# Optimization experiments

Hardware: AMD Instinct MI355X
Metric: run time of the kernel (lower is better)

The kernel has to match this reference:

```python
import jax, jax.numpy as jnp
import numpy as np

B, L, D, N, H = 2, 2048, 1024, 16, 64  # batch, seq, d_model, heads, head_dim


def setup_inputs() -> dict:
    key = jax.random.key(0)
    k_x, k_qkv, k_proj = jax.random.split(key, 3)
    x = jax.random.normal(k_x, (B, L, D), dtype=jnp.float32)
    # RoPE table (L, H//2, 2) holding (cos, sin) per position/frequency
    inv_freq = 1.0 / (10000.0 ** (jnp.arange(H // 2, dtype=jnp.float32) / (H // 2)))
    ang = jnp.arange(L, dtype=jnp.float32)[:, None] * inv_freq[None, :]  # (L, H//2)
    rope = jnp.stack([jnp.cos(ang), jnp.sin(ang)], axis=-1)  # (L, H//2, 2)
    mask = jnp.tril(jnp.ones((L, L), dtype=bool))[None, None]  # (1,1,L,L) causal
    w_qkv = jax.random.normal(k_qkv, (D, 3 * D), dtype=jnp.float32) * 0.02
    w_proj = jax.random.normal(k_proj, (D, D), dtype=jnp.float32) * 0.02
    return {"x": x, "rope": rope, "mask": mask, "w_qkv": w_qkv, "w_proj": w_proj}


def _apply_rope(t, rope):
    # t: (B, L, N, H), rope: (L, H//2, 2)
    b, l, n, h = t.shape
    tp = t.reshape(b, l, n, h // 2, 2)
    cos = rope[None, :, None, :, 0]  # (1, L, 1, H//2)
    sin = rope[None, :, None, :, 1]
    t0, t1 = tp[..., 0], tp[..., 1]
    out = jnp.stack([t0 * cos - t1 * sin, t0 * sin + t1 * cos], axis=-1)
    return out.reshape(b, l, n, h)


def reference(x, rope, mask, w_qkv, w_proj):
    b, l, d = x.shape
    h = rope.shape[1] * 2
    n = d // h
    qkv = x @ w_qkv  # (b, l, 3d)
    q, k, v = jnp.split(qkv, 3, axis=2)
    q = _apply_rope(q.reshape(b, l, n, h), rope)
    k = _apply_rope(k.reshape(b, l, n, h), rope)
    v = v.reshape(b, l, n, h)
    scale = 1.0 / jnp.sqrt(jnp.asarray(h, dtype=x.dtype))
    scores = jnp.einsum('blnh,bmnh->bnlm', q, k) * scale  # (b, n, l, l)
    scores = jnp.where(mask, scores, jnp.finfo(scores.dtype).min)
    attn = jax.nn.softmax(scores, axis=-1)
    out = jnp.einsum('bnlm,bmnh->blnh', attn, v).reshape(b, l, d)
    return out @ w_proj
```

## Files before the change

### kernel.cpp

```cpp
#include <hip/hip_runtime.h>
#include <cmath>
#include <cstdint>


typedef __attribute__((ext_vector_type(8))) short bfrag8;
typedef __attribute__((ext_vector_type(4))) float f32x4;
typedef __attribute__((ext_vector_type(8))) unsigned short u16x8;

#define AS1 __attribute__((address_space(1)))
#define AS3 __attribute__((address_space(3)))

__device__ __forceinline__ unsigned short f2bf(float f) {
  uint32_t u = __builtin_bit_cast(uint32_t, f);
  u += 0x7fffu + ((u >> 16) & 1u);
  return (unsigned short)(u >> 16);
}
__device__ __forceinline__ float bf2f(unsigned short h) {
  return __builtin_bit_cast(float, (uint32_t)h << 16);
}
__device__ __forceinline__ int swz(int row, int bytecol) {
  return row * 128 + (bytecol ^ ((row & 7) << 4));
}

__global__ __launch_bounds__(256)
void f32_to_bf16_vec(const float* __restrict__ in, unsigned short* __restrict__ out, int n) {
  const int i = (blockIdx.x * 256 + threadIdx.x) * 4;
  if (i < n) {
    float4 v = *reinterpret_cast<const float4*>(in + i);
    ushort4 o;
    o.x = f2bf(v.x); o.y = f2bf(v.y); o.z = f2bf(v.z); o.w = f2bf(v.w);
    *reinterpret_cast<ushort4*>(out + i) = o;
  }
}

__global__ __launch_bounds__(256)
void transpose_f32_to_bf16(const float* __restrict__ w, unsigned short* __restrict__ wT,
                           int R, int C) {
  __shared__ float t[32][33];
  const int tx = threadIdx.x & 31, ty = threadIdx.x >> 5;
  const int c0 = blockIdx.x * 32, r0 = blockIdx.y * 32;
  #pragma unroll
  for (int s = 0; s < 32; s += 8)
    t[ty + s][tx] = w[(size_t)(r0 + ty + s) * C + c0 + tx];
  __syncthreads();
  #pragma unroll
  for (int s = 0; s < 32; s += 8)
    wT[(size_t)(c0 + ty + s) * R + r0 + tx] = f2bf(t[tx][ty + s]);
}

template <int MODE>
__global__ __launch_bounds__(256)
void gemm_bt_bf16(const unsigned short* __restrict__ A, const unsigned short* __restrict__ Bt,
                  void* __restrict__ C0, unsigned short* __restrict__ C1,
                  unsigned short* __restrict__ Qr, unsigned short* __restrict__ Kr,
                  const float* __restrict__ rope, int K) {
  __shared__ __align__(16) unsigned short As[128 * 64];
  __shared__ __align__(16) unsigned short Bs[128 * 64];

  const int wg = blockIdx.x;
  const int szid = (wg & 7) * (gridDim.x >> 3) + (wg >> 3);
  const int brow = (szid & 31) * 128;
  const int bcol = (szid >> 5) * 128;

  const int tid  = threadIdx.x;
  const int wid  = tid >> 6, lane = tid & 63;
  const int wr = (wid >> 1) * 64;
  const int wc = (wid & 1) * 64;
  const int lrow = lane & 15;
  const int lko  = (lane >> 4) * 8;
  const int srow  = tid >> 3;
  const int skoff = (tid & 7) * 8;

  f32x4 acc[4][4];
  #pragma unroll
  for (int m = 0; m < 4; ++m)
    #pragma unroll
    for (int n = 0; n < 4; ++n) acc[m][n] = (f32x4){0.f, 0.f, 0.f, 0.f};

  for (int k0 = 0; k0 < K; k0 += 64) {
    __syncthreads();
    #pragma unroll
    for (int i = 0; i < 4; ++i) {
      const int r = i * 32 + srow;
      __builtin_amdgcn_global_load_lds(
          (const AS1 void*)(A + (size_t)(brow + r) * K + k0 + skoff),
          (AS3 void*)(As + r * 64 + skoff), 16, 0, 0);
      __builtin_amdgcn_global_load_lds(
          (const AS1 void*)(Bt + (size_t)(bcol + r) * K + k0 + skoff),
          (AS3 void*)(Bs + r * 64 + skoff), 16, 0, 0);
    }
    __syncthreads();

    #pragma unroll
    for (int ks = 0; ks < 2; ++ks) {
      bfrag8 a[4], b[4];
      #pragma unroll
      for (int m = 0; m < 4; ++m)
        a[m] = *reinterpret_cast<const bfrag8*>(&As[(wr + m * 16 + lrow) * 64 + ks * 32 + lko]);
      #pragma unroll
      for (int n = 0; n < 4; ++n)
        b[n] = *reinterpret_cast<const bfrag8*>(&Bs[(wc + n * 16 + lrow) * 64 + ks * 32 + lko]);
      #pragma unroll
      for (int m = 0; m < 4; ++m)
        #pragma unroll
        for (int n = 0; n < 4; ++n)
          acc[m][n] = __builtin_amdgcn_mfma_f32_16x16x32_bf16(a[m], b[n], acc[m][n], 0, 0, 0);
    }
  }

  const int crow0 = brow + wr + (lane >> 4) * 4;
  const int ccol0 = bcol + wc + lrow;

  if (MODE == 0) {
    float* C = (float*)C0;
    #pragma unroll
    for (int m = 0; m < 4; ++m)
      #pragma unroll
      for (int n = 0; n < 4; ++n)
        #pragma unroll
        for (int r = 0; r < 4; ++r)
          C[(size_t)(crow0 + m * 16 + r) * 1024 + ccol0 + n * 16] = acc[m][n][r];
  } else {
    if (bcol >= 2048) {
      const int cc = ccol0 - 2048;
      #pragma unroll
      for (int m = 0; m < 4; ++m)
        #pragma unroll
        for (int n = 0; n < 4; ++n)
          #pragma unroll
          for (int r = 0; r < 4; ++r)
            C1[(size_t)(crow0 + m * 16 + r) * 1024 + cc + n * 16] = f2bf(acc[m][n][r]);
    } else {
      const bool isq = (bcol < 1024);
      unsigned short* T = isq ? Qr : Kr;
      const int cb = bcol + wc + lrow - (isq ? 0 : 1024);
      const float sc = isq ? 0.125f : 1.0f;
      const int odd = lane & 1;
      const int pio = lrow >> 1;
      #pragma unroll
      for (int m = 0; m < 4; ++m) {
        #pragma unroll
        for (int r = 0; r < 4; ++r) {
          const int grow = crow0 + m * 16 + r;
          const float2* rrow = (const float2*)rope + (size_t)(grow & 2047) * 32;
          #pragma unroll
          for (int n = 0; n < 4; ++n) {
            const float v  = acc[m][n][r];
            const float pv = __shfl_xor(v, 1);
            const float2 cs = rrow[n * 8 + pio];
            const float o = odd ? fmaf(pv, cs.y, v * cs.x)
                                : fmaf(v, cs.x, -(pv * cs.y));
            T[(size_t)grow * 1024 + cb + n * 16] = f2bf(o * sc);
          }
        }
      }
    }
  }
}

__global__ __launch_bounds__(256)
void v_transpose_kernel(const unsigned short* __restrict__ Vbuf,
                        unsigned short* __restrict__ Vt) {
  __shared__ unsigned short t[64][72];
  const int lt = blockIdx.x;
  const int bn = blockIdx.y;
  const int b = bn >> 4, n = bn & 15;
  const int r = threadIdx.x >> 2;
  const int cb = (threadIdx.x & 3) << 4;

  const unsigned short* src = Vbuf + (size_t)b * 2048 * 1024 + n * 64;
  #pragma unroll
  for (int c = 0; c < 2; ++c) {
    u16x8 v = *reinterpret_cast<const u16x8*>(src + (size_t)(lt * 64 + r) * 1024 + cb + c * 8);
    *reinterpret_cast<u16x8*>(&t[r][cb + c * 8]) = v;
  }
  __syncthreads();
  unsigned short* dst = Vt + ((size_t)bn * 64 + r) * 2048 + lt * 64;
  #pragma unroll
  for (int c = 0; c < 2; ++c) {
    u16x8 o;
    #pragma unroll
    for (int j = 0; j < 8; ++j) o[j] = t[cb + c * 8 + j][r];
    *reinterpret_cast<u16x8*>(dst + cb + c * 8) = o;
  }
}

__global__ __launch_bounds__(256)
void attn_mfma_kernel(const unsigned short* __restrict__ Qr,
                      const unsigned short* __restrict__ Kr,
                      const unsigned short* __restrict__ Vt,
                      unsigned short* __restrict__ out) {
  __shared__ __align__(16) unsigned short PQ_s[64 * 64];
  __shared__ __align__(16) unsigned short K_s[2][64 * 64];
  __shared__ __align__(16) unsigned short V_s[2][64 * 64];

  const int tid = threadIdx.x;
  const int wid = tid >> 6, lane = tid & 63;
  const int lrow = lane & 15;
  const int lko  = (lane >> 4) * 8;
  const int i_blk = blockIdx.x;
  const int qt = (i_blk < 512) ? (31 - (i_blk >> 5)) : ((i_blk - 512) >> 5);
  const int bn = i_blk & 31;
  const int b = bn >> 4, n = bn & 15;

  const unsigned short* qb = Qr + (size_t)b * 2048 * 1024 + n * 64;
  const unsigned short* kb = Kr + (size_t)b * 2048 * 1024 + n * 64;
  const unsigned short* vb = Vt + (size_t)bn * 64 * 2048;
  unsigned short* ob = out + (size_t)b * 2048 * 1024 + n * 64;

  const int srow = lane >> 3;
  const int sgr  = (lane & 7) ^ srow;

  #pragma unroll
  for (int i = 0; i < 2; ++i) {
    const int row = i * 32 + wid * 8 + srow;
    __builtin_amdgcn_global_load_lds(
        (const AS1 void*)(qb + (size_t)(qt * 64 + row) * 1024 + sgr * 8),
        (AS3 void*)(PQ_s + (i * 32 + wid * 8) * 64 + lane * 8), 16, 0, 0);
    __builtin_amdgcn_global_load_lds(
        (const AS1 void*)(kb + (size_t)(0 * 64 + row) * 1024 + sgr * 8),
        (AS3 void*)(&K_s[0][(i * 32 + wid * 8) * 64 + lane * 8]), 16, 0, 0);
    __builtin_amdgcn_global_load_lds(
        (const AS1 void*)(vb + (size_t)row * 2048 + 0 * 64 + sgr * 8),
        (AS3 void*)(&V_s[0][(i * 32 + wid * 8) * 64 + lane * 8]), 16, 0, 0);
  }
  __syncthreads();

  bfrag8 aq[2];
  #pragma unroll
  for (int ks = 0; ks < 2; ++ks)
    aq[ks] = *reinterpret_cast<const bfrag8*>(
        (const char*)PQ_s + swz(wid * 16 + lrow, (ks * 32 + lko) * 2));

  f32x4 oa[4];
  float l_r[4];
  #pragma unroll
  for (int r = 0; r < 4; ++r) l_r[r] = 0.f;
  #pragma unroll
  for (int nn = 0; nn < 4; ++nn) oa[nn] = (f32x4){0.f, 0.f, 0.f, 0.f};

  int cur = 0;
  for (int kt = 0; kt <= qt; ++kt) {
    if (kt < qt) {
      #pragma unroll
      for (int i = 0; i < 2; ++i) {
        const int row = i * 32 + wid * 8 + srow;
        __builtin_amdgcn_global_load_lds(
            (const AS1 void*)(kb + (size_t)((kt + 1) * 64 + row) * 1024 + sgr * 8),
            (AS3 void*)(&K_s[cur ^ 1][(i * 32 + wid * 8) * 64 + lane * 8]), 16, 0, 0);
        __builtin_amdgcn_global_load_lds(
            (const AS1 void*)(vb + (size_t)row * 2048 + (kt + 1) * 64 + sgr * 8),
            (AS3 void*)(&V_s[cur ^ 1][(i * 32 + wid * 8) * 64 + lane * 8]), 16, 0, 0);
      }
    }
    const char* Kb = (const char*)&K_s[cur][0];
    const char* Vb = (const char*)&V_s[cur][0];

    f32x4 s[4];
    #pragma unroll
    for (int nn = 0; nn < 4; ++nn) s[nn] = (f32x4){0.f, 0.f, 0.f, 0.f};
    __builtin_amdgcn_s_setprio(1);
    #pragma unroll
    for (int ks = 0; ks < 2; ++ks) {
      #pragma unroll
      for (int nn = 0; nn < 4; ++nn) {
        bfrag8 bk = *reinterpret_cast<const bfrag8*>(Kb + swz(nn * 16 + lrow, (ks * 32 + lko) * 2));
        s[nn] = __builtin_amdgcn_mfma_f32_16x16x32_bf16(aq[ks], bk, s[nn], 0, 0, 0);
      }
    }
    __builtin_amdgcn_s_setprio(0);

    const bool diag = (kt == qt);
    #pragma unroll
    for (int r = 0; r < 4; ++r) {
      const int lrow_q = wid * 16 + (lane >> 4) * 4 + r;
      #pragma unroll
      for (int nn = 0; nn < 4; ++nn) {
        float v = s[nn][r];
        if (diag && (nn * 16 + lrow) > lrow_q) v = -INFINITY;
        const float p = __expf(v);
        const unsigned short pbf = f2bf(p);
        l_r[r] += bf2f(pbf);
        *(unsigned short*)((char*)PQ_s + swz(lrow_q, (nn * 16 + lrow) * 2)) = pbf;
      }
    }

    __builtin_amdgcn_s_setprio(1);
    #pragma unroll
    for (int ks = 0; ks < 2; ++ks) {
      bfrag8 pa = *reinterpret_cast<const bfrag8*>(
          (const char*)PQ_s + swz(wid * 16 + lrow, (ks * 32 + lko) * 2));
      #pragma unroll
      for (int nn = 0; nn < 4; ++nn) {
        bfrag8 bv = *reinterpret_cast<const bfrag8*>(Vb + swz(nn * 16 + lrow, (ks * 32 + lko) * 2));
        oa[nn] = __builtin_amdgcn_mfma_f32_16x16x32_bf16(pa, bv, oa[nn], 0, 0, 0);
      }
    }
    __builtin_amdgcn_s_setprio(0);

    __syncthreads();
    cur ^= 1;
  }

  unsigned short* op = ob + (size_t)(qt * 64 + wid * 16 + (lane >> 4) * 4) * 1024;
  #pragma unroll
  for (int r = 0; r < 4; ++r) {
    float rs = l_r[r];
    rs += __shfl_xor(rs, 1);
    rs += __shfl_xor(rs, 2);
    rs += __shfl_xor(rs, 4);
    rs += __shfl_xor(rs, 8);
    const float inv = 1.f / rs;
    #pragma unroll
    for (int nn = 0; nn < 4; ++nn)
      op[(size_t)r * 1024 + nn * 16 + lrow] = f2bf(oa[nn][r] * inv);
  }
}

extern "C" void kernel_launch(void* const* d_in, const int* in_sizes, int n_in,
                              void* d_out, int out_size, void* d_ws, size_t ws_size,
                              hipStream_t stream) {
  (void)in_sizes; (void)n_in; (void)out_size; (void)ws_size;
  const float* x      = (const float*)d_in[0];
  const float* rope   = (const float*)d_in[1];
  const float* w_qkv  = (const float*)d_in[3];
  const float* w_proj = (const float*)d_in[4];
  float* out = (float*)d_out;

  const size_t MB = 1u << 20;
  char* ws = (char*)d_ws;
  unsigned short* x_bf   = (unsigned short*)(ws);
  unsigned short* attn   = (unsigned short*)(ws);
  unsigned short* wqkvT  = (unsigned short*)(ws + 8 * MB);
  unsigned short* Qrp    = (unsigned short*)(ws + 14 * MB);
  unsigned short* Krp    = (unsigned short*)(ws + 22 * MB);
  unsigned short* Vbuf   = (unsigned short*)(ws + 30 * MB);
  unsigned short* Vtp    = (unsigned short*)(ws + 38 * MB);
  unsigned short* wprojT = (unsigned short*)(ws + 46 * MB);

  f32_to_bf16_vec<<<4096, 256, 0, stream>>>(x, x_bf, 4096 * 1024);
  transpose_f32_to_bf16<<<dim3(96, 32), 256, 0, stream>>>(w_qkv, wqkvT, 1024, 3072);
  transpose_f32_to_bf16<<<dim3(32, 32), 256, 0, stream>>>(w_proj, wprojT, 1024, 1024);

  gemm_bt_bf16<1><<<768, 256, 0, stream>>>(x_bf, wqkvT, nullptr, Vbuf,
                                           Qrp, Krp, rope, 1024);

  v_transpose_kernel<<<dim3(32, 32), 256, 0, stream>>>(Vbuf, Vtp);

  attn_mfma_kernel<<<1024, 256, 0, stream>>>(Qrp, Krp, Vtp, attn);

  gemm_bt_bf16<0><<<256, 256, 0, stream>>>(attn, wprojT, out, nullptr,
                                           nullptr, nullptr, nullptr, 1024);
}
```

Before: 225.2 us.

## Double-buffer GEMM LDS tiles, merge prep kernels, use 2D grid mapping

Three prep kernels (x cast plus two weight transposes) become one launch that dispatches on block index. The GEMM now double-buffers its A/B LDS tiles, issuing global-to-LDS loads for the next k-tile before computing on the current one. This is meant to hide load latency and leave one barrier per iteration. The swizzled 1D block mapping is replaced by a plain 2D grid, which may reduce L2 locality. LDS use doubles to 64KB per block, which can lower occupancy.

```diff
diff --git a/kernel.cpp b/kernel.cpp
--- a/kernel.cpp
+++ b/kernel.cpp
@@ -23,22 +23,33 @@
 }
 
 __global__ __launch_bounds__(256)
-void f32_to_bf16_vec(const float* __restrict__ in, unsigned short* __restrict__ out, int n) {
-  const int i = (blockIdx.x * 256 + threadIdx.x) * 4;
-  if (i < n) {
-    float4 v = *reinterpret_cast<const float4*>(in + i);
+void prep_kernel(const float* __restrict__ x, const float* __restrict__ w_qkv,
+                 const float* __restrict__ w_proj,
+                 unsigned short* __restrict__ x_bf, unsigned short* __restrict__ wqkvT,
+                 unsigned short* __restrict__ wprojT) {
+  __shared__ float t[32][33];
+  const int bid = blockIdx.x;
+  const int tid = threadIdx.x;
+
+  if (bid < 4096) {
+    const int i = (bid * 256 + tid) * 4;
+    float4 v = *reinterpret_cast<const float4*>(x + i);
     ushort4 o;
     o.x = f2bf(v.x); o.y = f2bf(v.y); o.z = f2bf(v.z); o.w = f2bf(v.w);
-    *reinterpret_cast<ushort4*>(out + i) = o;
-  }
-}
-
-__global__ __launch_bounds__(256)
-void transpose_f32_to_bf16(const float* __restrict__ w, unsigned short* __restrict__ wT,
-                           int R, int C) {
-  __shared__ float t[32][33];
-  const int tx = threadIdx.x & 31, ty = threadIdx.x >> 5;
-  const int c0 = blockIdx.x * 32, r0 = blockIdx.y * 32;
+    *reinterpret_cast<ushort4*>(x_bf + i) = o;
+    return;
+  }
+  const float* w;
+  unsigned short* wT;
+  int R, C, tb;
+  if (bid < 4096 + 3072) {
+    w = w_qkv; wT = wqkvT; R = 1024; C = 3072; tb = bid - 4096;
+  } else {
+    w = w_proj; wT = wprojT; R = 1024; C = 1024; tb = bid - 7168;
+  }
+  const int ntx = C >> 5;
+  const int c0 = (tb % ntx) * 32, r0 = (tb / ntx) * 32;
+  const int tx = tid & 31, ty = tid >> 5;
   #pragma unroll
   for (int s = 0; s < 32; s += 8)
     t[ty + s][tx] = w[(size_t)(r0 + ty + s) * C + c0 + tx];
@@ -54,14 +65,11 @@
                   void* __restrict__ C0, unsigned short* __restrict__ C1,
                   unsigned short* __restrict__ Qr, unsigned short* __restrict__ Kr,
                   const float* __restrict__ rope, int K) {
-  __shared__ __align__(16) unsigned short As[128 * 64];
-  __shared__ __align__(16) unsigned short Bs[128 * 64];
-
-  const int wg = blockIdx.x;
-  const int szid = (wg & 7) * (gridDim.x >> 3) + (wg >> 3);
-  const int brow = (szid & 31) * 128;
-  const int bcol = (szid >> 5) * 128;
-
+  __shared__ __align__(16) unsigned short As[2][128 * 64];
+  __shared__ __align__(16) unsigned short Bs[2][128 * 64];
+
+  const int brow = blockIdx.y * 128;
+  const int bcol = blockIdx.x * 128;
   const int tid  = threadIdx.x;
   const int wid  = tid >> 6, lane = tid & 63;
   const int wr = (wid >> 1) * 64;
@@ -77,35 +85,52 @@
     #pragma unroll
     for (int n = 0; n < 4; ++n) acc[m][n] = (f32x4){0.f, 0.f, 0.f, 0.f};
 
-  for (int k0 = 0; k0 < K; k0 += 64) {
-    __syncthreads();
-    #pragma unroll
-    for (int i = 0; i < 4; ++i) {
-      const int r = i * 32 + srow;
-      __builtin_amdgcn_global_load_lds(
-          (const AS1 void*)(A + (size_t)(brow + r) * K + k0 + skoff),
-          (AS3 void*)(As + r * 64 + skoff), 16, 0, 0);
-      __builtin_amdgcn_global_load_lds(
-          (const AS1 void*)(Bt + (size_t)(bcol + r) * K + k0 + skoff),
-          (AS3 void*)(Bs + r * 64 + skoff), 16, 0, 0);
-    }
-    __syncthreads();
+  const int nk = K >> 6;
+
+  #pragma unroll
+  for (int i = 0; i < 4; ++i) {
+    const int r = i * 32 + srow;
+    __builtin_amdgcn_global_load_lds(
+        (const AS1 void*)(A + (size_t)(brow + r) * K + skoff),
+        (AS3 void*)(&As[0][r * 64 + skoff]), 16, 0, 0);
+    __builtin_amdgcn_global_load_lds(
+        (const AS1 void*)(Bt + (size_t)(bcol + r) * K + skoff),
+        (AS3 void*)(&Bs[0][r * 64 + skoff]), 16, 0, 0);
+  }
+  __syncthreads();
+
+  for (int kt = 0; kt < nk; ++kt) {
+    const int cb = kt & 1;
+    if (kt + 1 < nk) {
+      const int k0 = (kt + 1) << 6;
+      #pragma unroll
+      for (int i = 0; i < 4; ++i) {
+        const int r = i * 32 + srow;
+        __builtin_amdgcn_global_load_lds(
+            (const AS1 void*)(A + (size_t)(brow + r) * K + k0 + skoff),
+            (AS3 void*)(&As[cb ^ 1][r * 64 + skoff]), 16, 0, 0);
+        __builtin_amdgcn_global_load_lds(
+            (const AS1 void*)(Bt + (size_t)(bcol + r) * K + k0 + skoff),
+            (AS3 void*)(&Bs[cb ^ 1][r * 64 + skoff]), 16, 0, 0);
+      }
+    }
 
     #pragma unroll
     for (int ks = 0; ks < 2; ++ks) {
       bfrag8 a[4], b[4];
       #pragma unroll
       for (int m = 0; m < 4; ++m)
-        a[m] = *reinterpret_cast<const bfrag8*>(&As[(wr + m * 16 + lrow) * 64 + ks * 32 + lko]);
+        a[m] = *reinterpret_cast<const bfrag8*>(&As[cb][(wr + m * 16 + lrow) * 64 + ks * 32 + lko]);
       #pragma unroll
       for (int n = 0; n < 4; ++n)
-        b[n] = *reinterpret_cast<const bfrag8*>(&Bs[(wc + n * 16 + lrow) * 64 + ks * 32 + lko]);
+        b[n] = *reinterpret_cast<const bfrag8*>(&Bs[cb][(wc + n * 16 + lrow) * 64 + ks * 32 + lko]);
       #pragma unroll
       for (int m = 0; m < 4; ++m)
         #pragma unroll
         for (int n = 0; n < 4; ++n)
           acc[m][n] = __builtin_amdgcn_mfma_f32_16x16x32_bf16(a[m], b[n], acc[m][n], 0, 0, 0);
     }
+    __syncthreads();
   }
 
   const int crow0 = brow + wr + (lane >> 4) * 4;
@@ -133,7 +158,7 @@
     } else {
       const bool isq = (bcol < 1024);
       unsigned short* T = isq ? Qr : Kr;
-      const int cb = bcol + wc + lrow - (isq ? 0 : 1024);
+      const int cb2 = bcol + wc + lrow - (isq ? 0 : 1024);
       const float sc = isq ? 0.125f : 1.0f;
       const int odd = lane & 1;
       const int pio = lrow >> 1;
@@ -150,7 +175,7 @@
             const float2 cs = rrow[n * 8 + pio];
             const float o = odd ? fmaf(pv, cs.y, v * cs.x)
                                 : fmaf(v, cs.x, -(pv * cs.y));
-            T[(size_t)grow * 1024 + cb + n * 16] = f2bf(o * sc);
+            T[(size_t)grow * 1024 + cb2 + n * 16] = f2bf(o * sc);
           }
         }
       }
@@ -338,17 +363,15 @@
   unsigned short* Vtp    = (unsigned short*)(ws + 38 * MB);
   unsigned short* wprojT = (unsigned short*)(ws + 46 * MB);
 
-  f32_to_bf16_vec<<<4096, 256, 0, stream>>>(x, x_bf, 4096 * 1024);
-  transpose_f32_to_bf16<<<dim3(96, 32), 256, 0, stream>>>(w_qkv, wqkvT, 1024, 3072);
-  transpose_f32_to_bf16<<<dim3(32, 32), 256, 0, stream>>>(w_proj, wprojT, 1024, 1024);
-
-  gemm_bt_bf16<1><<<768, 256, 0, stream>>>(x_bf, wqkvT, nullptr, Vbuf,
-                                           Qrp, Krp, rope, 1024);
+  prep_kernel<<<8192, 256, 0, stream>>>(x, w_qkv, w_proj, x_bf, wqkvT, wprojT);
+
+  gemm_bt_bf16<1><<<dim3(24, 32), 256, 0, stream>>>(x_bf, wqkvT, nullptr, Vbuf,
+                                                    Qrp, Krp, rope, 1024);
 
   v_transpose_kernel<<<dim3(32, 32), 256, 0, stream>>>(Vbuf, Vtp);
 
   attn_mfma_kernel<<<1024, 256, 0, stream>>>(Qrp, Krp, Vtp, attn);
 
-  gemm_bt_bf16<0><<<256, 256, 0, stream>>>(attn, wprojT, out, nullptr,
-                                           nullptr, nullptr, nullptr, 1024);
-}
+  gemm_bt_bf16<0><<<dim3(8, 32), 256, 0, stream>>>(attn, wprojT, out, nullptr,
+                                                   nullptr, nullptr, nullptr, 1024);
+}
```

After: 215.5 us. 1.04x faster.
